# Kernel optimization log

Hardware: AMD Instinct MI355X
Metric: run time of the kernel (lower is better)

## Reference

```python
import jax, jax.numpy as jnp
import numpy as np

N = 20000   # nodes
E = 160000  # edges
C = 512     # input_size / channels
D = 16      # edge_size
H = 256     # hidden_size
EPS = 1e-5  # BatchNorm eps (eval mode, init running stats: mean=0, var=1)


def setup_inputs() -> dict:
    key = jax.random.key(0)
    ks = jax.random.split(key, 24)
    w = lambda k, shape: (jax.random.normal(k, shape, jnp.float32) * 0.02)
    inp = {
        "x": jax.random.normal(ks[0], (N, C), jnp.float32),
        "edge_index": jax.random.randint(ks[1], (2, E), 0, N, jnp.int32),
        "edge_attr": jax.random.normal(ks[2], (E, D), jnp.float32),
        "goal_feat": jax.random.normal(ks[3], (N, C), jnp.float32),
        # CGConv 1
        "Wf1": w(ks[4], (2 * C + D, C)), "bf1": jnp.zeros((C,), jnp.float32),
        "Ws1": w(ks[5], (2 * C + D, C)), "bs1": jnp.zeros((C,), jnp.float32),
        "g1": jnp.ones((C,), jnp.float32), "be1": jnp.zeros((C,), jnp.float32),
        # CGConv 2
        "Wf2": w(ks[6], (2 * C + D, C)), "bf2": jnp.zeros((C,), jnp.float32),
        "Ws2": w(ks[7], (2 * C + D, C)), "bs2": jnp.zeros((C,), jnp.float32),
        "g2": jnp.ones((C,), jnp.float32), "be2": jnp.zeros((C,), jnp.float32),
        # GCNConv 3, 4
        "W3": w(ks[8], (C, H)), "b3": jnp.zeros((H,), jnp.float32),
        "W4": w(ks[9], (H, H)), "b4": jnp.zeros((H,), jnp.float32),
        # distance MLP: Lin(H+C -> C), ReLU, Lin(C -> 1)
        "Wd1": w(ks[10], (H + C, C)), "bd1": jnp.zeros((C,), jnp.float32),
        "Wd2": w(ks[11], (C, 1)), "bd2": jnp.zeros((1,), jnp.float32),
    }
    return inp


def cg_conv(x, src, dst, edge_attr, Wf, bf, Ws, bs, gamma, beta):
    # PyG CGConv: z = x_i || x_j || e;  m = sigmoid(lin_f(z)) * softplus(lin_s(z))
    # aggr='add' at targets, BatchNorm (eval, init stats), residual.
    z = jnp.concatenate([x[dst], x[src], edge_attr], axis=-1)  # [E, 2C+D]
    m = jax.nn.sigmoid(z @ Wf + bf) * jax.nn.softplus(z @ Ws + bs)  # [E, C]
    agg = jax.ops.segment_sum(m, dst, num_segments=N)  # [N, C]
    agg = agg * (gamma / jnp.sqrt(1.0 + EPS)) + beta   # BN eval (mean=0, var=1)
    return agg + x


def gcn_conv(x, src, dst, W, b):
    # PyG GCNConv with add_self_loops=True, normalize=True
    h = x @ W  # [N, out]
    loop = jnp.arange(N, dtype=src.dtype)
    s = jnp.concatenate([src, loop])
    d = jnp.concatenate([dst, loop])
    deg = jax.ops.segment_sum(jnp.ones_like(d, jnp.float32), d, num_segments=N)
    dinv = jnp.where(deg > 0, jax.lax.rsqrt(jnp.maximum(deg, 1.0)), 0.0)
    norm = dinv[s] * dinv[d]  # [E+N]
    out = jax.ops.segment_sum(norm[:, None] * h[s], d, num_segments=N)
    return out + b


def reference(x, edge_index, edge_attr, goal_feat,
              Wf1, bf1, Ws1, bs1, g1, be1,
              Wf2, bf2, Ws2, bs2, g2, be2,
              W3, b3, W4, b4, Wd1, bd1, Wd2, bd2):
    src = edge_index[0]  # x_j (source)
    dst = edge_index[1]  # x_i (target)
    h = jax.nn.relu(cg_conv(x, src, dst, edge_attr, Wf1, bf1, Ws1, bs1, g1, be1))
    h = jax.nn.relu(cg_conv(h, src, dst, edge_attr, Wf2, bf2, Ws2, bs2, g2, be2))
    h = jax.nn.relu(gcn_conv(h, src, dst, W3, b3))
    h = jax.nn.relu(gcn_conv(h, src, dst, W4, b4))
    z = jnp.concatenate([h, goal_feat], axis=1)  # [N, H+C]
    pred_dist = jax.nn.relu(z @ Wd1 + bd1) @ Wd2 + bd2  # [N, 1]
    return pred_dist, h
```

## Files before the change

kernel.cpp:

```cpp
#include <hip/hip_runtime.h>
#include <stdint.h>

#define NNODES 20000
#define NEDGES 160000
#define NPAD   20096

typedef float f32x4 __attribute__((ext_vector_type(4)));
typedef float f32x2 __attribute__((ext_vector_type(2)));
typedef short s16x8 __attribute__((ext_vector_type(8)));
typedef unsigned int u32x4 __attribute__((ext_vector_type(4)));
typedef _Float16 h16x2 __attribute__((ext_vector_type(2)));

__device__ __forceinline__ float b2f(unsigned short b) {
    unsigned int u = ((unsigned int)b) << 16;
    return __builtin_bit_cast(float, u);
}
__device__ __forceinline__ unsigned short f2b(float f) {
    unsigned int u = __builtin_bit_cast(unsigned int, f);
    unsigned int r = (u + 0x7FFFu + ((u >> 16) & 1u)) >> 16;
    return (unsigned short)r;
}
__device__ __forceinline__ f32x2 unpack2(unsigned int u) {
    f32x2 r;
    r.x = __builtin_bit_cast(float, u << 16);
    r.y = __builtin_bit_cast(float, u & 0xFFFF0000u);
    return r;
}
__device__ __forceinline__ unsigned int packh2(float a, float b) {
    h16x2 h = { (_Float16)a, (_Float16)b };
    return __builtin_bit_cast(unsigned int, h);
}
__device__ __forceinline__ float dot2h(unsigned int a, unsigned int b, float c) {
#if __has_builtin(__builtin_amdgcn_fdot2)
    return __builtin_amdgcn_fdot2(__builtin_bit_cast(h16x2, a),
                                  __builtin_bit_cast(h16x2, b), c, false);
#else
    float d;
    asm("v_dot2_f32_f16 %0, %1, %2, %3" : "=v"(d) : "v"(a), "v"(b), "v"(c));
    return d;
#endif
}

__global__ __launch_bounds__(256) void gemm_bt_kernel(
    const unsigned short* __restrict__ A,
    const unsigned short* __restrict__ BT,
    float* __restrict__ Cf,
    unsigned short* __restrict__ Cb,
    int M, int N, int K,
    const float* __restrict__ bias)
{
    __shared__ unsigned short As[128 * 64];
    __shared__ unsigned short Bs[128 * 64];
    const int tid  = threadIdx.x;
    const int wid  = tid >> 6;
    const int lane = tid & 63;
    const int bm = blockIdx.x * 128;
    const int bn = blockIdx.y * 128;
    const int wm = (wid & 1) * 64;
    const int wn = (wid >> 1) * 64;

    f32x4 acc[4][4];
#pragma unroll
    for (int i = 0; i < 4; i++)
#pragma unroll
        for (int j = 0; j < 4; j++) acc[i][j] = {0.f, 0.f, 0.f, 0.f};

    for (int k0 = 0; k0 < K; k0 += 64) {
#pragma unroll
        for (int r = 0; r < 4; r++) {
            int flat = r * 256 + tid;
            int row  = flat >> 3;
            int part = flat & 7;
            int pg   = part ^ (row & 7);
            const unsigned short* ga = A  + (size_t)(bm + row) * K + k0 + pg * 8;
            const unsigned short* gb = BT + (size_t)(bn + row) * K + k0 + pg * 8;
            __builtin_amdgcn_global_load_lds(
                (const __attribute__((address_space(1))) unsigned int*)ga,
                (__attribute__((address_space(3))) unsigned int*)&As[flat * 8], 16, 0, 0);
            __builtin_amdgcn_global_load_lds(
                (const __attribute__((address_space(1))) unsigned int*)gb,
                (__attribute__((address_space(3))) unsigned int*)&Bs[flat * 8], 16, 0, 0);
        }
        __syncthreads();

        const int kq8 = lane >> 4;
        const int rl  = lane & 15;
#pragma unroll
        for (int kk = 0; kk < 2; kk++) {
            s16x8 af[4], bfr[4];
#pragma unroll
            for (int mi = 0; mi < 4; mi++) {
                int row = wm + mi * 16 + rl;
                int slot = (kk * 4 + kq8) ^ (row & 7);
                af[mi] = *(const s16x8*)&As[row * 64 + slot * 8];
            }
#pragma unroll
            for (int ni = 0; ni < 4; ni++) {
                int row = wn + ni * 16 + rl;
                int slot = (kk * 4 + kq8) ^ (row & 7);
                bfr[ni] = *(const s16x8*)&Bs[row * 64 + slot * 8];
            }
#pragma unroll
            for (int mi = 0; mi < 4; mi++)
#pragma unroll
                for (int ni = 0; ni < 4; ni++)
                    acc[mi][ni] = __builtin_amdgcn_mfma_f32_16x16x32_bf16(
                        af[mi], bfr[ni], acc[mi][ni], 0, 0, 0);
        }
        __syncthreads();
    }

    const int cl = lane & 15;
    const int rq = (lane >> 4) * 4;
#pragma unroll
    for (int mi = 0; mi < 4; mi++)
#pragma unroll
        for (int ni = 0; ni < 4; ni++)
#pragma unroll
            for (int r = 0; r < 4; r++) {
                int row = bm + wm + mi * 16 + rq + r;
                int col = bn + wn + ni * 16 + cl;
                float v = acc[mi][ni][r];
                if (Cb) {
                    if (bias) v = fmaxf(v + bias[col], 0.f);
                    Cb[(size_t)row * N + col] = f2b(v);
                } else {
                    Cf[(size_t)row * N + col] = v;
                }
            }
}

__global__ void count_kernel(const int* __restrict__ ei, int* __restrict__ counts) {
    int e = blockIdx.x * blockDim.x + threadIdx.x;
    if (e < NEDGES) atomicAdd(&counts[ei[NEDGES + e]], 1);
}

__global__ __launch_bounds__(1024) void scan_kernel(const int* __restrict__ counts,
                                                    int* __restrict__ row_ptr)
{
    __shared__ int sdata[1024];
    const int t = threadIdx.x;
    int vals[20];
    const int base = t * 20;
    int lsum = 0;
#pragma unroll
    for (int j = 0; j < 20; j++) {
        int idx = base + j;
        int v = (idx < NNODES) ? counts[idx] : 0;
        vals[j] = v; lsum += v;
    }
    sdata[t] = lsum;
    __syncthreads();
    for (int off = 1; off < 1024; off <<= 1) {
        int v = (t >= off) ? sdata[t - off] : 0;
        __syncthreads();
        sdata[t] += v;
        __syncthreads();
    }
    int run = sdata[t] - lsum;
#pragma unroll
    for (int j = 0; j < 20; j++) {
        int idx = base + j;
        if (idx < NNODES) row_ptr[idx] = run;
        run += vals[j];
    }
    if (t == 1023) row_ptr[NNODES] = sdata[1023];
}

__global__ void fill_kernel(const int* __restrict__ ei,
                            const int* __restrict__ row_ptr,
                            int* __restrict__ cursor,
                            int* __restrict__ csr_src,
                            int* __restrict__ csr_eid)
{
    int e = blockIdx.x * blockDim.x + threadIdx.x;
    if (e >= NEDGES) return;
    int dst = ei[NEDGES + e];
    int p = row_ptr[dst] + atomicAdd(&cursor[dst], 1);
    csr_src[p] = ei[e];
    csr_eid[p] = e;
}

__global__ void dinv_kernel(const int* __restrict__ row_ptr, float* __restrict__ dinv) {
    int i = blockIdx.x * blockDim.x + threadIdx.x;
    if (i < NNODES) {
        int deg = row_ptr[i + 1] - row_ptr[i] + 1;
        dinv[i] = rsqrtf((float)deg);
    }
}

__global__ void pad_copy_kernel(const float* __restrict__ src,
                                unsigned short* __restrict__ dst,
                                int valid_rows, int cols, long total)
{
    long idx = (long)blockIdx.x * blockDim.x + threadIdx.x;
    if (idx >= total) return;
    int n = (int)(idx / cols);
    dst[idx] = (n < valid_rows) ? f2b(src[idx]) : (unsigned short)0;
}

__global__ void pack_cgw_kernel(const float* __restrict__ Wf,
                                const float* __restrict__ Ws,
                                unsigned short* __restrict__ out)
{
    int idx = blockIdx.x * blockDim.x + threadIdx.x;
    if (idx >= 2048 * 512) return;
    int j = idx >> 9;
    int k = idx & 511;
    int half = (j >= 1024);
    int jj = j & 1023;
    int c  = (jj >> 2) * 2 + (jj & 1);
    int fs = (jj >> 1) & 1;
    const float* W = fs ? Ws : Wf;
    float v = W[(size_t)(half ? 512 + k : k) * 512 + c];
    out[idx] = f2b(v);
}

__global__ void pack_t_kernel(const float* __restrict__ W,
                              unsigned short* __restrict__ WT,
                              int K, int Nout)
{
    long idx = (long)blockIdx.x * blockDim.x + threadIdx.x;
    if (idx >= (long)K * Nout) return;
    int j = (int)(idx / K);
    int k = (int)(idx % K);
    WT[idx] = f2b(W[(size_t)k * Nout + j]);
}

__global__ void pack_we_kernel(const float* __restrict__ Wf,
                               const float* __restrict__ Ws,
                               unsigned int* __restrict__ out)
{
    int idx = blockIdx.x * blockDim.x + threadIdx.x;
    if (idx >= 8192) return;
    int q  = idx & 3;
    int c2 = (idx >> 2) & 255;
    int k  = idx >> 10;
    const float* W = (q >> 1) ? Ws : Wf;
    int c = c2 * 2 + (q & 1);
    float v0 = W[(size_t)(1024 + 2 * k) * 512 + c];
    float v1 = W[(size_t)(1024 + 2 * k + 1) * 512 + c];
    out[idx] = packh2(v0, v1);
}

__global__ void pack_ea_kernel(const int* __restrict__ csr_eid,
                               const float* __restrict__ ea,
                               unsigned int* __restrict__ out)
{
    int idx = blockIdx.x * blockDim.x + threadIdx.x;
    if (idx >= NEDGES * 8) return;
    int i = idx >> 3;
    int j = idx & 7;
    int eid = csr_eid[i];
    out[idx] = packh2(ea[(size_t)eid * 16 + 2 * j], ea[(size_t)eid * 16 + 2 * j + 1]);
}

#define CG_NPB 4

#define CG_LOADE(q_, a0_, a1_, idx) do {                                       \
    int sx_ = __builtin_amdgcn_readfirstlane(csr_src[idx]);                    \
    q_  = *(const uint2*)(P + (size_t)sx_ * 2048 + 1024 + c0 * 2);             \
    a0_ = eapk[(size_t)(idx) * 2];                                             \
    a1_ = eapk[(size_t)(idx) * 2 + 1];                                         \
} while (0)

#define CG_COMP(q_, a0_, a1_) do {                                             \
    float f0 = baseF.x, f1 = baseF.y, s0 = baseS.x, s1 = baseS.y;              \
    _Pragma("unroll")                                                          \
    for (int k = 0; k < 4; k++) {                                              \
        f0 = dot2h(a0_[k], w[k][0], f0);                                       \
        f1 = dot2h(a0_[k], w[k][1], f1);                                       \
        s0 = dot2h(a0_[k], w[k][2], s0);                                       \
        s1 = dot2h(a0_[k], w[k][3], s1);                                       \
    }                                                                          \
    _Pragma("unroll")                                                          \
    for (int k = 0; k < 4; k++) {                                              \
        f0 = dot2h(a1_[k], w[4 + k][0], f0);                                   \
        f1 = dot2h(a1_[k], w[4 + k][1], f1);                                   \
        s0 = dot2h(a1_[k], w[4 + k][2], s0);                                   \
        s1 = dot2h(a1_[k], w[4 + k][3], s1);                                   \
    }                                                                          \
    f32x2 pf = unpack2(q_.x);                                                  \
    f32x2 ps = unpack2(q_.y);                                                  \
    f0 += pf.x; f1 += pf.y; s0 += ps.x; s1 += ps.y;                            \
    float sp0 = __logf(1.f + __expf(s0));                                      \
    float sp1 = __logf(1.f + __expf(s1));                                      \
    float sg0 = __builtin_amdgcn_rcpf(1.f + __expf(-f0));                      \
    float sg1 = __builtin_amdgcn_rcpf(1.f + __expf(-f1));                      \
    acc.x = fmaf(sp0, sg0, acc.x);                                             \
    acc.y = fmaf(sp1, sg1, acc.y);                                             \
} while (0)

__global__ __launch_bounds__(256, 1) void cg_gather_kernel(
    const unsigned short* __restrict__ P,
    const int* __restrict__ row_ptr,
    const int* __restrict__ csr_src,
    const u32x4* __restrict__ wE,
    const u32x4* __restrict__ eapk,
    const float* __restrict__ bfv,
    const float* __restrict__ bsv,
    const float* __restrict__ g,
    const float* __restrict__ be,
    const float* __restrict__ xresf,
    const unsigned short* __restrict__ xresb,
    unsigned short* __restrict__ hout)
{
    const int tid = threadIdx.x;
    const int c0  = tid * 2;
    const int nbase = blockIdx.x * CG_NPB;

    u32x4 w[8];
#pragma unroll
    for (int k = 0; k < 8; k++) w[k] = wE[k * 256 + tid];

    const f32x2 bfx = *(const f32x2*)&bfv[c0];
    const f32x2 bsx = *(const f32x2*)&bsv[c0];
    const f32x2 gv  = *(const f32x2*)&g[c0];
    const f32x2 bev = *(const f32x2*)&be[c0];
    const float rs = rsqrtf(1.f + 1e-5f);

    for (int n = nbase; n < nbase + CG_NPB; n++) {
        if (n >= NNODES) {
            *(unsigned int*)&hout[(size_t)n * 512 + c0] = 0;
            continue;
        }
        const unsigned short* Pd = P + (size_t)n * 2048;
        const uint2 qb = *(const uint2*)(Pd + c0 * 2);
        const f32x2 baseF = unpack2(qb.x) + bfx;
        const f32x2 baseS = unpack2(qb.y) + bsx;

        f32x2 acc = {0.f, 0.f};
        const int i0 = row_ptr[n], i1 = row_ptr[n + 1];

        if (i0 < i1) {
            uint2 qA = {}, qB = {}, qC = {};
            u32x4 aA0 = {}, aA1 = {}, aB0 = {}, aB1 = {}, aC0 = {}, aC1 = {};
            CG_LOADE(qA, aA0, aA1, i0);
            if (i0 + 1 < i1) CG_LOADE(qB, aB0, aB1, i0 + 1);
            if (i0 + 2 < i1) CG_LOADE(qC, aC0, aC1, i0 + 2);
            int i = i0;
            while (true) {
                CG_COMP(qA, aA0, aA1);
                if (i + 3 < i1) CG_LOADE(qA, aA0, aA1, i + 3);
                if (++i >= i1) break;
                CG_COMP(qB, aB0, aB1);
                if (i + 3 < i1) CG_LOADE(qB, aB0, aB1, i + 3);
                if (++i >= i1) break;
                CG_COMP(qC, aC0, aC1);
                if (i + 3 < i1) CG_LOADE(qC, aC0, aC1, i + 3);
                if (++i >= i1) break;
            }
        }

        f32x2 res;
        if (xresf) {
            res = *(const f32x2*)&xresf[(size_t)n * 512 + c0];
        } else {
            res = unpack2(*(const unsigned int*)&xresb[(size_t)n * 512 + c0]);
        }
        float v0 = fmaxf(acc.x * (gv.x * rs) + bev.x + res.x, 0.f);
        float v1 = fmaxf(acc.y * (gv.y * rs) + bev.y + res.y, 0.f);
        unsigned int packed = (unsigned int)f2b(v0) | ((unsigned int)f2b(v1) << 16);
        *(unsigned int*)&hout[(size_t)n * 512 + c0] = packed;
    }
}

__global__ __launch_bounds__(256) void gcn_gather_kernel(
    const unsigned short* __restrict__ pre,
    const int* __restrict__ row_ptr,
    const int* __restrict__ csr_src,
    const float* __restrict__ dinv,
    const float* __restrict__ b,
    unsigned short* __restrict__ hout,
    float* __restrict__ doutf)
{
    const int tid  = threadIdx.x;
    const int lane = tid & 63;
    const int n = blockIdx.x * 4 + (tid >> 6);
    const int c = lane * 4;
    if (n >= NNODES) {
        if (n < NPAD) { uint2 z = {0u, 0u}; *(uint2*)&hout[(size_t)n * 256 + c] = z; }
        return;
    }
    const float din = dinv[n];
    f32x4 acc = {0.f, 0.f, 0.f, 0.f};
    const int i0 = row_ptr[n], i1 = row_ptr[n + 1];

#define GCN_LOADE(dv_, pv_, idx) do {                                          \
    int sx_ = __builtin_amdgcn_readfirstlane(csr_src[idx]);                    \
    dv_ = dinv[sx_];                                                           \
    pv_ = *(const uint2*)&pre[(size_t)sx_ * 256 + c];                          \
} while (0)

#define GCN_COMP(dv_, pv_) do {                                                \
    f32x2 p0 = unpack2(pv_.x);                                                 \
    f32x2 p1 = unpack2(pv_.y);                                                 \
    acc.x = fmaf(dv_, p0.x, acc.x);                                            \
    acc.y = fmaf(dv_, p0.y, acc.y);                                            \
    acc.z = fmaf(dv_, p1.x, acc.z);                                            \
    acc.w = fmaf(dv_, p1.y, acc.w);                                            \
} while (0)

    if (i0 < i1) {
        float dvA = 0.f, dvB = 0.f, dvC = 0.f;
        uint2 pvA = {}, pvB = {}, pvC = {};
        GCN_LOADE(dvA, pvA, i0);
        if (i0 + 1 < i1) GCN_LOADE(dvB, pvB, i0 + 1);
        if (i0 + 2 < i1) GCN_LOADE(dvC, pvC, i0 + 2);
        int i = i0;
        while (true) {
            GCN_COMP(dvA, pvA);
            if (i + 3 < i1) GCN_LOADE(dvA, pvA, i + 3);
            if (++i >= i1) break;
            GCN_COMP(dvB, pvB);
            if (i + 3 < i1) GCN_LOADE(dvB, pvB, i + 3);
            if (++i >= i1) break;
            GCN_COMP(dvC, pvC);
            if (i + 3 < i1) GCN_LOADE(dvC, pvC, i + 3);
            if (++i >= i1) break;
        }
    }
    uint2 sv = *(const uint2*)&pre[(size_t)n * 256 + c];
    f32x2 s0 = unpack2(sv.x);
    f32x2 s1 = unpack2(sv.y);
    const f32x4 bv = *(const f32x4*)&b[c];
    const float d2 = din * din;
    float v0 = fmaxf(fmaf(acc.x, din, d2 * s0.x) + bv.x, 0.f);
    float v1 = fmaxf(fmaf(acc.y, din, d2 * s0.y) + bv.y, 0.f);
    float v2 = fmaxf(fmaf(acc.z, din, d2 * s1.x) + bv.z, 0.f);
    float v3 = fmaxf(fmaf(acc.w, din, d2 * s1.y) + bv.w, 0.f);
    uint2 o;
    o.x = (unsigned int)f2b(v0) | ((unsigned int)f2b(v1) << 16);
    o.y = (unsigned int)f2b(v2) | ((unsigned int)f2b(v3) << 16);
    *(uint2*)&hout[(size_t)n * 256 + c] = o;
    if (doutf) {
        f32x4 vv = {v0, v1, v2, v3};
        *(f32x4*)&doutf[(size_t)n * 256 + c] = vv;
    }
}

__global__ void build_zc_kernel(const unsigned short* __restrict__ h4,
                                const float* __restrict__ goal,
                                unsigned short* __restrict__ zc)
{
    long idx = (long)blockIdx.x * blockDim.x + threadIdx.x;
    if (idx >= (long)NPAD * 768) return;
    int n = (int)(idx / 768);
    int c = (int)(idx % 768);
    unsigned short v = 0;
    if (n < NNODES)
        v = (c < 256) ? h4[(size_t)n * 256 + c]
                      : f2b(goal[(size_t)n * 512 + (c - 256)]);
    zc[idx] = v;
}

__global__ __launch_bounds__(256) void final_dot_kernel(
    const unsigned short* __restrict__ t,
    const float* __restrict__ Wd2,
    const float* __restrict__ bd2,
    float* __restrict__ pred)
{
    const int lane = threadIdx.x & 63;
    const int wid  = threadIdx.x >> 6;
    float w[8];
#pragma unroll
    for (int i = 0; i < 8; i++) w[i] = Wd2[lane * 8 + i];
    const float bd = bd2[0];
    for (int n = blockIdx.x * 4 + wid; n < NNODES; n += gridDim.x * 4) {
        const unsigned short* tp = t + (size_t)n * 512 + lane * 8;
        float s = 0.f;
#pragma unroll
        for (int i = 0; i < 8; i++) s = fmaf(b2f(tp[i]), w[i], s);
#pragma unroll
        for (int off = 32; off; off >>= 1) s += __shfl_xor(s, off, 64);
        if (lane == 0) pred[n] = s + bd;
    }
}

extern "C" void kernel_launch(void* const* d_in, const int* in_sizes, int n_in,
                              void* d_out, int out_size, void* d_ws, size_t ws_size,
                              hipStream_t stream)
{
    (void)in_sizes; (void)n_in; (void)out_size; (void)ws_size;
    const float* x    = (const float*)d_in[0];
    const int*   ei   = (const int*)d_in[1];
    const float* ea   = (const float*)d_in[2];
    const float* goal = (const float*)d_in[3];
    const float* Wf1  = (const float*)d_in[4];
    const float* bf1  = (const float*)d_in[5];
    const float* Ws1  = (const float*)d_in[6];
    const float* bs1  = (const float*)d_in[7];
    const float* g1   = (const float*)d_in[8];
    const float* be1  = (const float*)d_in[9];
    const float* Wf2  = (const float*)d_in[10];
    const float* bf2  = (const float*)d_in[11];
    const float* Ws2  = (const float*)d_in[12];
    const float* bs2  = (const float*)d_in[13];
    const float* g2   = (const float*)d_in[14];
    const float* be2  = (const float*)d_in[15];
    const float* W3   = (const float*)d_in[16];
    const float* b3   = (const float*)d_in[17];
    const float* W4   = (const float*)d_in[18];
    const float* b4   = (const float*)d_in[19];
    const float* Wd1  = (const float*)d_in[20];
    const float* bd1  = (const float*)d_in[21];
    const float* Wd2  = (const float*)d_in[22];
    const float* bd2  = (const float*)d_in[23];
    float* outp = (float*)d_out;

    char* ws = (char*)d_ws;
    size_t off = 0;
    auto alloc = [&](size_t bytes) -> char* {
        char* p = ws + off;
        off += (bytes + 255) & ~(size_t)255;
        return p;
    };
    unsigned short* P     = (unsigned short*)alloc((size_t)NPAD * 2048 * 2);
    unsigned short* bufA  = (unsigned short*)alloc((size_t)NPAD * 512 * 2);
    unsigned short* bufB  = (unsigned short*)alloc((size_t)NPAD * 512 * 2);
    unsigned short* bufC  = (unsigned short*)alloc((size_t)NPAD * 512 * 2);
    unsigned short* wpack = (unsigned short*)alloc((size_t)2048 * 512 * 2);
    int*            counts  = (int*)alloc((size_t)NNODES * 4);
    int*            row_ptr = (int*)alloc((size_t)(NNODES + 1) * 4);
    int*            csr_src = (int*)alloc((size_t)NEDGES * 4);
    int*            csr_eid = (int*)alloc((size_t)NEDGES * 4);
    float*          dinv    = (float*)alloc((size_t)NNODES * 4);
    unsigned int*   wEbuf   = (unsigned int*)alloc((size_t)8192 * 4);
    unsigned int*   eapk    = (unsigned int*)alloc((size_t)NEDGES * 8 * 4);

    unsigned short* xpad  = bufA;
    unsigned short* h1    = bufB;
    unsigned short* h2    = bufA;
    unsigned short* pre_b = bufB;
    unsigned short* h3    = bufC;
    unsigned short* h4    = bufA;
    unsigned short* zc    = P;
    unsigned short* tb    = P + (size_t)NPAD * 1024;

    const int B = 256;

    hipMemsetAsync(counts, 0, (size_t)NNODES * 4, stream);
    count_kernel<<<(NEDGES + B - 1) / B, B, 0, stream>>>(ei, counts);
    scan_kernel<<<1, 1024, 0, stream>>>(counts, row_ptr);
    hipMemsetAsync(counts, 0, (size_t)NNODES * 4, stream);
    fill_kernel<<<(NEDGES + B - 1) / B, B, 0, stream>>>(ei, row_ptr, counts, csr_src, csr_eid);
    dinv_kernel<<<(NNODES + B - 1) / B, B, 0, stream>>>(row_ptr, dinv);
    pack_ea_kernel<<<(NEDGES * 8 + B - 1) / B, B, 0, stream>>>(csr_eid, ea, eapk);

    {
        long tot = (long)NPAD * 512;
        pad_copy_kernel<<<(unsigned)((tot + B - 1) / B), B, 0, stream>>>(x, xpad, NNODES, 512, tot);
    }

    dim3 gBig(NPAD / 128, 2048 / 128);

    pack_cgw_kernel<<<(2048 * 512 + B - 1) / B, B, 0, stream>>>(Wf1, Ws1, wpack);
    pack_we_kernel<<<(8192 + B - 1) / B, B, 0, stream>>>(Wf1, Ws1, wEbuf);
    gemm_bt_kernel<<<gBig, B, 0, stream>>>(xpad, wpack, nullptr, P, NPAD, 2048, 512, nullptr);
    cg_gather_kernel<<<NPAD / CG_NPB, B, 0, stream>>>(P, row_ptr, csr_src,
                                                      (const u32x4*)wEbuf, (const u32x4*)eapk,
                                                      bf1, bs1, g1, be1,
                                                      x, nullptr, h1);

    pack_cgw_kernel<<<(2048 * 512 + B - 1) / B, B, 0, stream>>>(Wf2, Ws2, wpack);
    gemm_bt_kernel<<<gBig, B, 0, stream>>>(h1, wpack, nullptr, P, NPAD, 2048, 512, nullptr);
    pack_we_kernel<<<(8192 + B - 1) / B, B, 0, stream>>>(Wf2, Ws2, wEbuf);
    cg_gather_kernel<<<NPAD / CG_NPB, B, 0, stream>>>(P, row_ptr, csr_src,
                                                      (const u32x4*)wEbuf, (const u32x4*)eapk,
                                                      bf2, bs2, g2, be2,
                                                      nullptr, h1, h2);

    pack_t_kernel<<<(256 * 512 + B - 1) / B, B, 0, stream>>>(W3, wpack, 512, 256);
    gemm_bt_kernel<<<dim3(NPAD / 128, 2), B, 0, stream>>>(h2, wpack, nullptr, pre_b, NPAD, 256, 512, nullptr);
    gcn_gather_kernel<<<NPAD / 4, B, 0, stream>>>(pre_b, row_ptr, csr_src, dinv, b3, h3, (float*)nullptr);

    pack_t_kernel<<<(256 * 256 + B - 1) / B, B, 0, stream>>>(W4, wpack, 256, 256);
    gemm_bt_kernel<<<dim3(NPAD / 128, 2), B, 0, stream>>>(h3, wpack, nullptr, pre_b, NPAD, 256, 256, nullptr);
    gcn_gather_kernel<<<NPAD / 4, B, 0, stream>>>(pre_b, row_ptr, csr_src, dinv, b4, h4, outp + NNODES);

    build_zc_kernel<<<(unsigned)(((long)NPAD * 768 + B - 1) / B), B, 0, stream>>>(h4, goal, zc);
    pack_t_kernel<<<(512 * 768 + B - 1) / B, B, 0, stream>>>(Wd1, wpack, 768, 512);
    gemm_bt_kernel<<<dim3(NPAD / 128, 4), B, 0, stream>>>(zc, wpack, nullptr, tb, NPAD, 512, 768, bd1);
    final_dot_kernel<<<512, B, 0, stream>>>(tb, Wd2, bd2, outp);
}
```

Baseline: 813.1 us.

## Prescale CGConv weights by log2(e) and use native exp2/log2 in gather

New measurement: 784.1 us. 1.04x faster.

```diff
diff --git a/kernel.cpp b/kernel.cpp
--- a/kernel.cpp
+++ b/kernel.cpp
@@ -10,6 +10,9 @@
 typedef short s16x8 __attribute__((ext_vector_type(8)));
 typedef unsigned int u32x4 __attribute__((ext_vector_type(4)));
 typedef _Float16 h16x2 __attribute__((ext_vector_type(2)));
+
+#define L2E 1.44269504088896340736f
+#define LN2 0.6931471805599453f
 
 __device__ __forceinline__ float b2f(unsigned short b) {
     unsigned int u = ((unsigned int)b) << 16;
@@ -38,6 +41,20 @@
     float d;
     asm("v_dot2_f32_f16 %0, %1, %2, %3" : "=v"(d) : "v"(a), "v"(b), "v"(c));
     return d;
+#endif
+}
+__device__ __forceinline__ float exp2f_fast(float x) {
+#if __has_builtin(__builtin_amdgcn_exp2f)
+    return __builtin_amdgcn_exp2f(x);
+#else
+    return __builtin_exp2f(x);
+#endif
+}
+__device__ __forceinline__ float log2f_fast(float x) {
+#if __has_builtin(__builtin_amdgcn_logf)
+    return __builtin_amdgcn_logf(x);
+#else
+    return __builtin_log2f(x);
 #endif
 }
 
@@ -212,7 +229,7 @@
     int c  = (jj >> 2) * 2 + (jj & 1);
     int fs = (jj >> 1) & 1;
     const float* W = fs ? Ws : Wf;
-    float v = W[(size_t)(half ? 512 + k : k) * 512 + c];
+    float v = W[(size_t)(half ? 512 + k : k) * 512 + c] * L2E;
     out[idx] = f2b(v);
 }
 
@@ -233,13 +250,14 @@
 {
     int idx = blockIdx.x * blockDim.x + threadIdx.x;
     if (idx >= 8192) return;
-    int q  = idx & 3;
-    int c2 = (idx >> 2) & 255;
-    int k  = idx >> 10;
+    int tid = idx >> 5;
+    int r   = idx & 31;
+    int k   = r >> 2;
+    int q   = r & 3;
     const float* W = (q >> 1) ? Ws : Wf;
-    int c = c2 * 2 + (q & 1);
-    float v0 = W[(size_t)(1024 + 2 * k) * 512 + c];
-    float v1 = W[(size_t)(1024 + 2 * k + 1) * 512 + c];
+    int c = tid * 2 + (q & 1);
+    float v0 = W[(size_t)(1024 + 2 * k) * 512 + c] * L2E;
+    float v1 = W[(size_t)(1024 + 2 * k + 1) * 512 + c] * L2E;
     out[idx] = packh2(v0, v1);
 }
 
@@ -283,10 +301,10 @@
     f32x2 pf = unpack2(q_.x);                                                  \
     f32x2 ps = unpack2(q_.y);                                                  \
     f0 += pf.x; f1 += pf.y; s0 += ps.x; s1 += ps.y;                            \
-    float sp0 = __logf(1.f + __expf(s0));                                      \
-    float sp1 = __logf(1.f + __expf(s1));                                      \
-    float sg0 = __builtin_amdgcn_rcpf(1.f + __expf(-f0));                      \
-    float sg1 = __builtin_amdgcn_rcpf(1.f + __expf(-f1));                      \
+    float sp0 = log2f_fast(1.f + exp2f_fast(s0));                              \
+    float sp1 = log2f_fast(1.f + exp2f_fast(s1));                              \
+    float sg0 = __builtin_amdgcn_rcpf(1.f + exp2f_fast(-f0));                  \
+    float sg1 = __builtin_amdgcn_rcpf(1.f + exp2f_fast(-f1));                  \
     acc.x = fmaf(sp0, sg0, acc.x);                                             \
     acc.y = fmaf(sp1, sg1, acc.y);                                             \
 } while (0)
@@ -295,7 +313,7 @@
     const unsigned short* __restrict__ P,
     const int* __restrict__ row_ptr,
     const int* __restrict__ csr_src,
-    const u32x4* __restrict__ wE,
+    const unsigned int* __restrict__ wE,
     const u32x4* __restrict__ eapk,
     const float* __restrict__ bfv,
     const float* __restrict__ bsv,
@@ -309,15 +327,29 @@
     const int c0  = tid * 2;
     const int nbase = blockIdx.x * CG_NPB;
 
-    u32x4 w[8];
-#pragma unroll
-    for (int k = 0; k < 8; k++) w[k] = wE[k * 256 + tid];
-
-    const f32x2 bfx = *(const f32x2*)&bfv[c0];
-    const f32x2 bsx = *(const f32x2*)&bsv[c0];
+    const unsigned int* wp = wE + (size_t)tid * 32;
+    u32x4 w0, w1, w2, w3, w4, w5, w6, w7;
+    asm volatile(
+        "global_load_dwordx4 %0, %8, off\n\t"
+        "global_load_dwordx4 %1, %8, off offset:16\n\t"
+        "global_load_dwordx4 %2, %8, off offset:32\n\t"
+        "global_load_dwordx4 %3, %8, off offset:48\n\t"
+        "global_load_dwordx4 %4, %8, off offset:64\n\t"
+        "global_load_dwordx4 %5, %8, off offset:80\n\t"
+        "global_load_dwordx4 %6, %8, off offset:96\n\t"
+        "global_load_dwordx4 %7, %8, off offset:112\n\t"
+        "s_waitcnt vmcnt(0)"
+        : "=&v"(w0), "=&v"(w1), "=&v"(w2), "=&v"(w3),
+          "=&v"(w4), "=&v"(w5), "=&v"(w6), "=&v"(w7)
+        : "v"(wp));
+    __builtin_amdgcn_sched_barrier(0);
+    const u32x4 w[8] = {w0, w1, w2, w3, w4, w5, w6, w7};
+
+    const f32x2 bfx = *(const f32x2*)&bfv[c0] * L2E;
+    const f32x2 bsx = *(const f32x2*)&bsv[c0] * L2E;
     const f32x2 gv  = *(const f32x2*)&g[c0];
     const f32x2 bev = *(const f32x2*)&be[c0];
-    const float rs = rsqrtf(1.f + 1e-5f);
+    const float rsl = rsqrtf(1.f + 1e-5f) * LN2;
 
     for (int n = nbase; n < nbase + CG_NPB; n++) {
         if (n >= NNODES) {
@@ -333,21 +365,17 @@
         const int i0 = row_ptr[n], i1 = row_ptr[n + 1];
 
         if (i0 < i1) {
-            uint2 qA = {}, qB = {}, qC = {};
-            u32x4 aA0 = {}, aA1 = {}, aB0 = {}, aB1 = {}, aC0 = {}, aC1 = {};
+            uint2 qA = {}, qB = {};
+            u32x4 aA0 = {}, aA1 = {}, aB0 = {}, aB1 = {};
             CG_LOADE(qA, aA0, aA1, i0);
             if (i0 + 1 < i1) CG_LOADE(qB, aB0, aB1, i0 + 1);
-            if (i0 + 2 < i1) CG_LOADE(qC, aC0, aC1, i0 + 2);
             int i = i0;
             while (true) {
                 CG_COMP(qA, aA0, aA1);
-                if (i + 3 < i1) CG_LOADE(qA, aA0, aA1, i + 3);
+                if (i + 2 < i1) CG_LOADE(qA, aA0, aA1, i + 2);
                 if (++i >= i1) break;
                 CG_COMP(qB, aB0, aB1);
-                if (i + 3 < i1) CG_LOADE(qB, aB0, aB1, i + 3);
-                if (++i >= i1) break;
-                CG_COMP(qC, aC0, aC1);
-                if (i + 3 < i1) CG_LOADE(qC, aC0, aC1, i + 3);
+                if (i + 2 < i1) CG_LOADE(qB, aB0, aB1, i + 2);
                 if (++i >= i1) break;
             }
         }
@@ -358,8 +386,8 @@
         } else {
             res = unpack2(*(const unsigned int*)&xresb[(size_t)n * 512 + c0]);
         }
-        float v0 = fmaxf(acc.x * (gv.x * rs) + bev.x + res.x, 0.f);
-        float v1 = fmaxf(acc.y * (gv.y * rs) + bev.y + res.y, 0.f);
+        float v0 = fmaxf(acc.x * (gv.x * rsl) + bev.x + res.x, 0.f);
+        float v1 = fmaxf(acc.y * (gv.y * rsl) + bev.y + res.y, 0.f);
         unsigned int packed = (unsigned int)f2b(v0) | ((unsigned int)f2b(v1) << 16);
         *(unsigned int*)&hout[(size_t)n * 512 + c0] = packed;
     }
@@ -558,7 +586,7 @@
     pack_we_kernel<<<(8192 + B - 1) / B, B, 0, stream>>>(Wf1, Ws1, wEbuf);
     gemm_bt_kernel<<<gBig, B, 0, stream>>>(xpad, wpack, nullptr, P, NPAD, 2048, 512, nullptr);
     cg_gather_kernel<<<NPAD / CG_NPB, B, 0, stream>>>(P, row_ptr, csr_src,
-                                                      (const u32x4*)wEbuf, (const u32x4*)eapk,
+                                                      wEbuf, (const u32x4*)eapk,
                                                       bf1, bs1, g1, be1,
                                                       x, nullptr, h1);
 
@@ -566,7 +594,7 @@
     gemm_bt_kernel<<<gBig, B, 0, stream>>>(h1, wpack, nullptr, P, NPAD, 2048, 512, nullptr);
     pack_we_kernel<<<(8192 + B - 1) / B, B, 0, stream>>>(Wf2, Ws2, wEbuf);
     cg_gather_kernel<<<NPAD / CG_NPB, B, 0, stream>>>(P, row_ptr, csr_src,
-                                                      (const u32x4*)wEbuf, (const u32x4*)eapk,
+                                                      wEbuf, (const u32x4*)eapk,
                                                       bf2, bs2, g2, be2,
                                                       nullptr, h1, h2);
 
```
